# Kernel optimization log

Hardware: AMD Instinct MI355X
Metric: run time of the kernel (lower is better)

Reference implementation:

```python
import jax, jax.numpy as jnp
import numpy as np

D = H = W = 128  # voxel grid resolution (shape = [1,1,128,128,128] in source)
N = 2_000_000    # number of points


def splat(vals, pts, d, h, w):
    """Adjoint of trilinear F.grid_sample (align_corners=False, zeros padding).
    vals: [N] point values; pts: [N,3] normalized (x,y,z) coords in [-1,1].
    Returns [d,h,w] voxel grid with trilinear scatter-add of vals.
    """
    # unnormalize: pixel = ((coord+1)*size - 1) / 2  (align_corners=False)
    x = ((pts[:, 0] + 1.0) * w - 1.0) * 0.5
    y = ((pts[:, 1] + 1.0) * h - 1.0) * 0.5
    z = ((pts[:, 2] + 1.0) * d - 1.0) * 0.5
    x0 = jnp.floor(x); y0 = jnp.floor(y); z0 = jnp.floor(z)
    fx = x - x0; fy = y - y0; fz = z - z0
    x0i = x0.astype(jnp.int32); y0i = y0.astype(jnp.int32); z0i = z0.astype(jnp.int32)
    grid = jnp.zeros((d * h * w,), dtype=vals.dtype)
    for dz in (0, 1):
        wz = fz if dz else (1.0 - fz)
        for dy in (0, 1):
            wy = fy if dy else (1.0 - fy)
            for dx in (0, 1):
                wx = fx if dx else (1.0 - fx)
                xi = x0i + dx; yi = y0i + dy; zi = z0i + dz
                valid = (xi >= 0) & (xi < w) & (yi >= 0) & (yi < h) & (zi >= 0) & (zi < d)
                idx = jnp.where(valid, (zi * h + yi) * w + xi, 0)
                contrib = jnp.where(valid, wx * wy * wz * vals, 0.0)
                grid = grid.at[idx].add(contrib)
    return grid.reshape(d, h, w)


def huber_sum(pred, gt, delta=1.0):
    diff = pred - gt
    a = jnp.abs(diff)
    return jnp.sum(jnp.where(a <= delta, 0.5 * diff * diff, delta * (a - 0.5 * delta)))


def setup_inputs() -> dict:
    key = jax.random.key(0)
    k1, k2, k3 = jax.random.split(key, 3)
    coords = jax.random.uniform(k1, (1, N, 3), jnp.float32, -0.95, 0.95)
    registration_pred = 0.02 * jax.random.normal(k2, (1, N, 3), jnp.float32)
    registration_gt = 0.02 * jax.random.normal(k3, (1, N, 3), jnp.float32)
    return {"registration_pred": registration_pred,
            "registration_gt": registration_gt,
            "coords": coords}


def reference(registration_pred, registration_gt, coords):
    pred_pts = (coords + registration_pred).reshape(-1, 3)   # [N,3]
    gt_pts = (coords + registration_gt).reshape(-1, 3)       # [N,3]
    vals = jnp.ones((pred_pts.shape[0],), dtype=coords.dtype)
    pred_rast = splat(vals, pred_pts, D, H, W)   # [128,128,128]
    gt_rast = splat(vals, gt_pts, D, H, W)       # [128,128,128]
    return huber_sum(pred_rast, gt_rast)
```

## Files before the change

kernel.cpp:

```cpp
#include <hip/hip_runtime.h>
#include <stdint.h>

constexpr int GRID_R = 128;
constexpr int NVOX = GRID_R * GRID_R * GRID_R;

constexpr int TILE = 16;
constexpr int TPD = GRID_R / TILE;
constexpr int NBINS = TPD * TPD * TPD;
constexpr int CAP = 12288;
constexpr int CUR_STRIDE = 16;
constexpr size_t CUR_BYTES = (size_t)NBINS * CUR_STRIDE * sizeof(uint32_t);
constexpr size_t ITEMS_BYTES = (size_t)NBINS * CAP * sizeof(uint2);
constexpr size_t SORT_WS_NEEDED = CUR_BYTES + ITEMS_BYTES;

constexpr int PAD = 18;

constexpr int QXB = 9;
constexpr int QZSTRIDE = QXB * QXB;
constexpr int QARR = PAD * QZSTRIDE;
constexpr float QSCALE = 1024.0f;

__device__ __forceinline__ int axis_tiles(int c0, int* ts, int* ls) {
    int n = 0;
    if ((unsigned)c0 < (unsigned)GRID_R) {
        int tx = c0 >> 4; ts[0] = tx; ls[0] = c0 - (tx << 4); n = 1;
    }
    int c1 = c0 + 1;
    if ((unsigned)c1 < (unsigned)GRID_R) {
        int tx = c1 >> 4;
        if (!n || tx != ts[0]) { ts[n] = tx; ls[n] = c0 - (tx << 4); ++n; }
    }
    return n;
}

template <typename F>
__device__ __forceinline__ void for_each_replica(float px, float py, float pz,
                                                 uint32_t g, F&& emit) {
    float x0f = floorf(px), y0f = floorf(py), z0f = floorf(pz);
    int x0 = (int)x0f, y0 = (int)y0f, z0 = (int)z0f;
    float fx = px - x0f, fy = py - y0f, fz = pz - z0f;

    int txs[2], lxs[2], tys[2], lys[2], tzs[2], lzs[2];
    int ntx = axis_tiles(x0, txs, lxs);
    int nty = axis_tiles(y0, tys, lys);
    int ntz = axis_tiles(z0, tzs, lzs);
    if (!ntx || !nty || !ntz) return;

    uint32_t ufx = (uint32_t)(fx * 65535.0f + 0.5f);
    uint32_t ufy = (uint32_t)(fy * 65535.0f + 0.5f);
    uint32_t ufz = (uint32_t)(fz * 65535.0f + 0.5f);
    uint32_t w0 = ufx | (ufy << 16);

    for (int c = 0; c < ntz; ++c)
        for (int b = 0; b < nty; ++b)
            for (int a = 0; a < ntx; ++a) {
                int bin = (tzs[c] * TPD + tys[b]) * TPD + txs[a];
                uint32_t w1 = ufz |
                              ((uint32_t)(lxs[a] + 1) << 16) |
                              ((uint32_t)(lys[b] + 1) << 21) |
                              ((uint32_t)(lzs[c] + 1) << 26) |
                              (g << 31);
                emit(bin, w0, w1);
            }
}

__device__ __forceinline__ void load_pts(const float* __restrict__ pred_reg,
                                         const float* __restrict__ gt_reg,
                                         const float* __restrict__ coords,
                                         int i, float* pa, float* pb) {
    float cx = coords[3 * i + 0], cy = coords[3 * i + 1], cz = coords[3 * i + 2];
    pa[0] = (cx + pred_reg[3 * i + 0] + 1.0f) * 64.0f - 0.5f;
    pa[1] = (cy + pred_reg[3 * i + 1] + 1.0f) * 64.0f - 0.5f;
    pa[2] = (cz + pred_reg[3 * i + 2] + 1.0f) * 64.0f - 0.5f;
    pb[0] = (cx + gt_reg[3 * i + 0] + 1.0f) * 64.0f - 0.5f;
    pb[1] = (cy + gt_reg[3 * i + 1] + 1.0f) * 64.0f - 0.5f;
    pb[2] = (cz + gt_reg[3 * i + 2] + 1.0f) * 64.0f - 0.5f;
}

#define SBLOCK 1024
#define PPT 8

__global__ __launch_bounds__(SBLOCK, 8) void scatter_kernel(
        const float* __restrict__ pred_reg, const float* __restrict__ gt_reg,
        const float* __restrict__ coords, uint32_t* __restrict__ cursors,
        uint2* __restrict__ items, int n) {
    __shared__ uint32_t h[NBINS];
    __shared__ uint32_t base[NBINS];
    int t = threadIdx.x;
    for (int b = t; b < NBINS; b += SBLOCK) h[b] = 0;
    __syncthreads();

    int i0 = blockIdx.x * (SBLOCK * PPT);

    for (int k = 0; k < PPT; ++k) {
        int i = i0 + k * SBLOCK + t;
        if (i >= n) break;
        float pa[3], pb[3];
        load_pts(pred_reg, gt_reg, coords, i, pa, pb);
        auto cnt = [&](int bin, uint32_t, uint32_t) { atomicAdd(&h[bin], 1u); };
        for_each_replica(pa[0], pa[1], pa[2], 0u, cnt);
        for_each_replica(pb[0], pb[1], pb[2], 1u, cnt);
    }
    __syncthreads();

    for (int b = t; b < NBINS; b += SBLOCK) {
        uint32_t c = h[b];
        base[b] = c ? atomicAdd(&cursors[b * CUR_STRIDE], c) : 0u;
        h[b] = 0;
    }
    __syncthreads();

    for (int k = 0; k < PPT; ++k) {
        int i = i0 + k * SBLOCK + t;
        if (i >= n) break;
        float pa[3], pb[3];
        load_pts(pred_reg, gt_reg, coords, i, pa, pb);
        auto put = [&](int bin, uint32_t w0, uint32_t w1) {
            uint32_t r = atomicAdd(&h[bin], 1u);
            uint32_t s = base[bin] + r;
            if (s < (uint32_t)CAP)
                items[(size_t)bin * CAP + s] = make_uint2(w0, w1);
        };
        for_each_replica(pa[0], pa[1], pa[2], 0u, put);
        for_each_replica(pb[0], pb[1], pb[2], 1u, put);
    }
}

#define ABLOCK 1024

__device__ __forceinline__ void accum_item(uint64_t* __restrict__ U,
                                           uint32_t wx, uint32_t wy) {
    float fx = (float)(wx & 0xffffu) * (1.0f / 65535.0f);
    float fy = (float)(wx >> 16) * (1.0f / 65535.0f);
    float fz = (float)(wy & 0xffffu) * (1.0f / 65535.0f);
    int lx1 = (int)((wy >> 16) & 31u);
    int ly1 = (int)((wy >> 21) & 31u);
    int lz1 = (int)((wy >> 26) & 31u);
    uint32_t g = wy >> 31;

    int px = lx1 & 1, xb = lx1 >> 1;
    int py = ly1 & 1, yb = ly1 >> 1;
    uint64_t* arr = U + ((g << 2) | (py << 1) | px) * QARR;
    int idx = lz1 * QZSTRIDE + yb * QXB + xb;

    float wx1 = fx, wx0 = 1.0f - fx;
    float wy1 = fy, wy0 = 1.0f - fy;
    float q00 = wx0 * wy0 * QSCALE, q10 = wx1 * wy0 * QSCALE;
    float q01 = wx0 * wy1 * QSCALE, q11 = wx1 * wy1 * QSCALE;
    float wz1 = fz, wz0 = 1.0f - fz;

    auto pk = [&](float wz) -> uint64_t {
        uint32_t lo = (uint32_t)(q00 * wz + 0.5f) |
                      ((uint32_t)(q10 * wz + 0.5f) << 16);
        uint32_t hi = (uint32_t)(q01 * wz + 0.5f) |
                      ((uint32_t)(q11 * wz + 0.5f) << 16);
        return (uint64_t)lo | ((uint64_t)hi << 32);
    };
    atomicAdd((unsigned long long*)&arr[idx],
              (unsigned long long)pk(wz0));
    atomicAdd((unsigned long long*)&arr[idx + QZSTRIDE],
              (unsigned long long)pk(wz1));
}

__global__ __launch_bounds__(ABLOCK, 4) void accum_kernel(
        const uint2* __restrict__ items, const uint32_t* __restrict__ cursors,
        float* __restrict__ out) {
    __shared__ uint64_t U[8 * QARR];
    __shared__ float wsum[ABLOCK / 64];
    int bin = blockIdx.x, t = threadIdx.x;

    for (int j = t; j < 8 * QARR; j += ABLOCK) U[j] = 0ull;
    __syncthreads();

    uint32_t cnt = cursors[bin * CUR_STRIDE];
    if (cnt > (uint32_t)CAP) cnt = CAP;
    const uint2* seg = items + (size_t)bin * CAP;
    const uint4* seg4 = (const uint4*)seg;
    uint32_t npair = cnt >> 1;

    uint32_t i = t;
    uint4 w = (i < npair) ? seg4[i] : make_uint4(0, 0, 0, 0);
    while (i < npair) {
        uint32_t inext = i + ABLOCK;
        uint4 wn = (inext < npair) ? seg4[inext] : make_uint4(0, 0, 0, 0);
        accum_item(U, w.x, w.y);
        accum_item(U, w.z, w.w);
        w = wn; i = inext;
    }
    if ((cnt & 1) && t == 0) {
        uint2 lw = seg[cnt - 1];
        accum_item(U, lw.x, lw.y);
    }
    __syncthreads();

    float s = 0.0f;
    for (int j = t; j < TILE * TILE * TILE; j += ABLOCK) {
        int x = (j & 15) + 1, y = ((j >> 4) & 15) + 1, z = (j >> 8) + 1;
        float v[2];
#pragma unroll
        for (int g = 0; g < 2; ++g) {
            float acc = 0.0f;
#pragma unroll
            for (int py = 0; py < 2; ++py)
#pragma unroll
                for (int px = 0; px < 2; ++px) {
                    int xb = (x - px) >> 1, lx = (x - px) & 1;
                    int yb = (y - py) >> 1, ly = (y - py) & 1;
                    uint64_t q = U[((g << 2) | (py << 1) | px) * QARR +
                                   z * QZSTRIDE + yb * QXB + xb];
                    acc += (float)((uint32_t)(q >> (((ly << 1) | lx) << 4)) &
                                   0xFFFFu);
                }
            v[g] = acc;
        }
        float d = (v[0] - v[1]) * (1.0f / QSCALE);
        float aa = fabsf(d);
        s += (aa <= 1.0f) ? 0.5f * d * d : (aa - 0.5f);
    }
#pragma unroll
    for (int off = 32; off > 0; off >>= 1) s += __shfl_down(s, off, 64);
    int lane = t & 63, wid = t >> 6;
    if (!lane) wsum[wid] = s;
    __syncthreads();
    if (!t) {
        float tot = 0.0f;
#pragma unroll
        for (int wv = 0; wv < ABLOCK / 64; ++wv) tot += wsum[wv];
        unsafeAtomicAdd(out, tot);
    }
}

__device__ __forceinline__ void splat_point(float nx, float ny, float nz,
                                            float* __restrict__ grid) {
    float x = (nx + 1.0f) * 64.0f - 0.5f;
    float y = (ny + 1.0f) * 64.0f - 0.5f;
    float z = (nz + 1.0f) * 64.0f - 0.5f;
    float x0f = floorf(x), y0f = floorf(y), z0f = floorf(z);
    float fx = x - x0f, fy = y - y0f, fz = z - z0f;
    int x0 = (int)x0f, y0 = (int)y0f, z0 = (int)z0f;
    int xs[2] = {x0, x0 + 1}, ys[2] = {y0, y0 + 1}, zs[2] = {z0, z0 + 1};
    float wxs[2] = {1.0f - fx, fx}, wys[2] = {1.0f - fy, fy}, wzs[2] = {1.0f - fz, fz};
#pragma unroll
    for (int dz = 0; dz < 2; ++dz) {
        int zi = zs[dz]; if ((unsigned)zi >= (unsigned)GRID_R) continue;
#pragma unroll
        for (int dy = 0; dy < 2; ++dy) {
            int yi = ys[dy]; if ((unsigned)yi >= (unsigned)GRID_R) continue;
            float wzy = wzs[dz] * wys[dy];
            int basei = (zi * GRID_R + yi) * GRID_R;
#pragma unroll
            for (int dx = 0; dx < 2; ++dx) {
                int xi = xs[dx]; if ((unsigned)xi >= (unsigned)GRID_R) continue;
                unsafeAtomicAdd(&grid[basei + xi], wzy * wxs[dx]);
            }
        }
    }
}

__global__ void splat_kernel(const float* __restrict__ pred_reg,
                             const float* __restrict__ gt_reg,
                             const float* __restrict__ coords,
                             float* __restrict__ gridA, float* __restrict__ gridB,
                             int n) {
    int i = blockIdx.x * blockDim.x + threadIdx.x;
    if (i >= n) return;
    float cx = coords[3 * i + 0], cy = coords[3 * i + 1], cz = coords[3 * i + 2];
    splat_point(cx + pred_reg[3 * i + 0], cy + pred_reg[3 * i + 1],
                cz + pred_reg[3 * i + 2], gridA);
    splat_point(cx + gt_reg[3 * i + 0], cy + gt_reg[3 * i + 1],
                cz + gt_reg[3 * i + 2], gridB);
}

__global__ void huber_kernel(const float4* __restrict__ A,
                             const float4* __restrict__ B,
                             float* __restrict__ out) {
    int i = blockIdx.x * blockDim.x + threadIdx.x;
    float4 a = A[i], b = B[i];
    auto h1 = [](float d) { float x = fabsf(d);
                            return (x <= 1.0f) ? 0.5f * d * d : (x - 0.5f); };
    float s = h1(a.x - b.x) + h1(a.y - b.y) + h1(a.z - b.z) + h1(a.w - b.w);
#pragma unroll
    for (int off = 32; off > 0; off >>= 1) s += __shfl_down(s, off, 64);
    __shared__ float wsum[4];
    int lane = threadIdx.x & 63, wid = threadIdx.x >> 6;
    if (!lane) wsum[wid] = s;
    __syncthreads();
    if (!threadIdx.x) atomicAdd(out, wsum[0] + wsum[1] + wsum[2] + wsum[3]);
}

extern "C" void kernel_launch(void* const* d_in, const int* in_sizes, int n_in,
                              void* d_out, int out_size, void* d_ws, size_t ws_size,
                              hipStream_t stream) {
    const float* pred_reg = (const float*)d_in[0];
    const float* gt_reg   = (const float*)d_in[1];
    const float* coords   = (const float*)d_in[2];
    float* outp = (float*)d_out;
    int n = in_sizes[2] / 3;

    hipMemsetAsync(d_out, 0, sizeof(float), stream);

    if (ws_size >= SORT_WS_NEEDED) {
        uint32_t* cursors = (uint32_t*)d_ws;
        uint2* items = (uint2*)((char*)d_ws + CUR_BYTES);
        hipMemsetAsync(cursors, 0, CUR_BYTES, stream);

        int sblocks = (n + SBLOCK * PPT - 1) / (SBLOCK * PPT);
        scatter_kernel<<<sblocks, SBLOCK, 0, stream>>>(pred_reg, gt_reg, coords,
                                                       cursors, items, n);
        accum_kernel<<<NBINS, ABLOCK, 0, stream>>>(items, cursors, outp);
    } else {
        float* gridA = (float*)d_ws;
        float* gridB = gridA + NVOX;
        hipMemsetAsync(d_ws, 0, (size_t)2 * NVOX * sizeof(float), stream);
        int blocks = (n + 255) / 256;
        splat_kernel<<<blocks, 256, 0, stream>>>(pred_reg, gt_reg, coords,
                                                 gridA, gridB, n);
        huber_kernel<<<NVOX / 4 / 256, 256, 0, stream>>>((const float4*)gridA,
                                                         (const float4*)gridB, outp);
    }
}
```

Before: 170.9 us.

## Replace two-pass count/scatter binning with single-pass shared ring buffers flushed in groups

The scatter kernel no longer reads points twice (count pass then put pass). Each bin now gets a small shared-memory ring, and full groups of 8 items are flushed to global memory with one cursor atomic per group. Partial groups are padded with sentinel items, which the accumulation step skips, and bin capacity is raised to hold the padding. This removes the second point load and the per-block histogram pass, at the cost of extra syncs per iteration, global atomics on ring overflow, and lower occupancy from the larger shared-memory footprint.

```diff
diff --git a/kernel.cpp b/kernel.cpp
--- a/kernel.cpp
+++ b/kernel.cpp
@@ -7,11 +7,13 @@
 constexpr int TILE = 16;
 constexpr int TPD = GRID_R / TILE;
 constexpr int NBINS = TPD * TPD * TPD;
-constexpr int CAP = 12288;
+constexpr int CAP = 13312;
 constexpr int CUR_STRIDE = 16;
 constexpr size_t CUR_BYTES = (size_t)NBINS * CUR_STRIDE * sizeof(uint32_t);
 constexpr size_t ITEMS_BYTES = (size_t)NBINS * CAP * sizeof(uint2);
 constexpr size_t SORT_WS_NEEDED = CUR_BYTES + ITEMS_BYTES;
+
+constexpr uint32_t SENT_W1 = 0xFFFFFFFFu;
 
 constexpr int PAD = 18;
 
@@ -79,50 +81,83 @@
 
 #define SBLOCK 1024
 #define PPT 8
-
-__global__ __launch_bounds__(SBLOCK, 8) void scatter_kernel(
+constexpr int RCAP = 16;
+
+__global__ __launch_bounds__(SBLOCK) void scatter_kernel(
         const float* __restrict__ pred_reg, const float* __restrict__ gt_reg,
         const float* __restrict__ coords, uint32_t* __restrict__ cursors,
         uint2* __restrict__ items, int n) {
-    __shared__ uint32_t h[NBINS];
-    __shared__ uint32_t base[NBINS];
+    __shared__ uint2 ring[NBINS * RCAP];
+    __shared__ uint32_t pc[NBINS];
+    __shared__ uint32_t fl[NBINS];
     int t = threadIdx.x;
-    for (int b = t; b < NBINS; b += SBLOCK) h[b] = 0;
+    if (t < NBINS) { pc[t] = 0; fl[t] = 0; }
     __syncthreads();
 
     int i0 = blockIdx.x * (SBLOCK * PPT);
 
     for (int k = 0; k < PPT; ++k) {
         int i = i0 + k * SBLOCK + t;
-        if (i >= n) break;
-        float pa[3], pb[3];
-        load_pts(pred_reg, gt_reg, coords, i, pa, pb);
-        auto cnt = [&](int bin, uint32_t, uint32_t) { atomicAdd(&h[bin], 1u); };
-        for_each_replica(pa[0], pa[1], pa[2], 0u, cnt);
-        for_each_replica(pb[0], pb[1], pb[2], 1u, cnt);
-    }
-    __syncthreads();
-
-    for (int b = t; b < NBINS; b += SBLOCK) {
-        uint32_t c = h[b];
-        base[b] = c ? atomicAdd(&cursors[b * CUR_STRIDE], c) : 0u;
-        h[b] = 0;
-    }
-    __syncthreads();
-
-    for (int k = 0; k < PPT; ++k) {
-        int i = i0 + k * SBLOCK + t;
-        if (i >= n) break;
-        float pa[3], pb[3];
-        load_pts(pred_reg, gt_reg, coords, i, pa, pb);
-        auto put = [&](int bin, uint32_t w0, uint32_t w1) {
-            uint32_t r = atomicAdd(&h[bin], 1u);
-            uint32_t s = base[bin] + r;
-            if (s < (uint32_t)CAP)
-                items[(size_t)bin * CAP + s] = make_uint2(w0, w1);
-        };
-        for_each_replica(pa[0], pa[1], pa[2], 0u, put);
-        for_each_replica(pb[0], pb[1], pb[2], 1u, put);
+        if (i < n) {
+            float pa[3], pb[3];
+            load_pts(pred_reg, gt_reg, coords, i, pa, pb);
+            auto emit = [&](int bin, uint32_t w0, uint32_t w1) {
+                uint32_t base = fl[bin] * 8u;
+                uint32_t r = atomicAdd(&pc[bin], 1u);
+                if (r - base < (uint32_t)RCAP) {
+                    ring[bin * RCAP + (int)(r & (RCAP - 1))] = make_uint2(w0, w1);
+                } else {
+                    atomicSub(&pc[bin], 1u);
+                    uint32_t s = atomicAdd(&cursors[bin * CUR_STRIDE], 1u);
+                    if (s < (uint32_t)CAP)
+                        items[(size_t)bin * CAP + s] = make_uint2(w0, w1);
+                }
+            };
+            for_each_replica(pa[0], pa[1], pa[2], 0u, emit);
+            for_each_replica(pb[0], pb[1], pb[2], 1u, emit);
+        }
+        __syncthreads();
+        if (t < NBINS) {
+            uint32_t f = fl[t], p = pc[t];
+            uint32_t ng = (p - f * 8u) >> 3;
+            if (ng) {
+                uint32_t s0 = atomicAdd(&cursors[t * CUR_STRIDE], ng * 8u);
+                for (uint32_t g = 0; g < ng; ++g) {
+                    uint32_t sb = s0 + g * 8u;
+                    int rb = t * RCAP + (int)(((f + g) & 1u) << 3);
+                    uint2* dst = items + (size_t)t * CAP + sb;
+                    if (sb + 8u <= (uint32_t)CAP) {
+#pragma unroll
+                        for (int j = 0; j < 8; ++j) dst[j] = ring[rb + j];
+                    } else {
+                        for (int j = 0; j < 8; ++j)
+                            if (sb + j < (uint32_t)CAP) dst[j] = ring[rb + j];
+                    }
+                }
+                fl[t] = f + ng;
+            }
+        }
+        __syncthreads();
+    }
+
+    if (t < NBINS) {
+        uint32_t f = fl[t], p = pc[t];
+        uint32_t res = p - f * 8u;
+        if (res) {
+            for (uint32_t j = res; j < 8u; ++j)
+                ring[t * RCAP + (int)((f * 8u + j) & (RCAP - 1))] =
+                    make_uint2(0u, SENT_W1);
+            uint32_t s0 = atomicAdd(&cursors[t * CUR_STRIDE], 8u);
+            int rb = t * RCAP + (int)((f & 1u) << 3);
+            uint2* dst = items + (size_t)t * CAP + s0;
+            if (s0 + 8u <= (uint32_t)CAP) {
+#pragma unroll
+                for (int j = 0; j < 8; ++j) dst[j] = ring[rb + j];
+            } else {
+                for (int j = 0; j < 8; ++j)
+                    if (s0 + j < (uint32_t)CAP) dst[j] = ring[rb + j];
+            }
+        }
     }
 }
 
@@ -130,10 +165,11 @@
 
 __device__ __forceinline__ void accum_item(uint64_t* __restrict__ U,
                                            uint32_t wx, uint32_t wy) {
+    int lx1 = (int)((wy >> 16) & 31u);
+    if (lx1 == 31) return;
     float fx = (float)(wx & 0xffffu) * (1.0f / 65535.0f);
     float fy = (float)(wx >> 16) * (1.0f / 65535.0f);
     float fz = (float)(wy & 0xffffu) * (1.0f / 65535.0f);
-    int lx1 = (int)((wy >> 16) & 31u);
     int ly1 = (int)((wy >> 21) & 31u);
     int lz1 = (int)((wy >> 26) & 31u);
     uint32_t g = wy >> 31;
```

Measured after the change: 169.2 us. Within noise of the previous version (-1.0%).

## Stage scatter writes through per-bin LDS ring buffers for coalesced 64-byte flushes

Applied to the files above, without the earlier changes.

The binning scatter kernel now buffers items in a 16-entry shared-memory ring per bin and flushes full groups of 8 items as 64-byte vector stores, instead of each thread doing a scattered 8-byte global store. Per-bin reservations are rounded up to multiples of 16, and leftover slots are padded with sentinel items that the accumulate kernel skips. Ring overflow goes to a small per-bin spill region read separately. This aims to cut write inefficiency from scattered stores, at the cost of extra block-wide barriers per PPT iteration, more shared memory (lower occupancy), larger capacity and sentinel padding traffic.

```diff
diff --git a/kernel.cpp b/kernel.cpp
--- a/kernel.cpp
+++ b/kernel.cpp
@@ -7,11 +7,15 @@
 constexpr int TILE = 16;
 constexpr int TPD = GRID_R / TILE;
 constexpr int NBINS = TPD * TPD * TPD;
-constexpr int CAP = 12288;
+constexpr int CAP = 13312;
+constexpr int SPILL_CAP = 64;
+constexpr int CAPM = CAP - SPILL_CAP;
 constexpr int CUR_STRIDE = 16;
 constexpr size_t CUR_BYTES = (size_t)NBINS * CUR_STRIDE * sizeof(uint32_t);
 constexpr size_t ITEMS_BYTES = (size_t)NBINS * CAP * sizeof(uint2);
 constexpr size_t SORT_WS_NEEDED = CUR_BYTES + ITEMS_BYTES;
+
+constexpr uint32_t SENT_W1 = 0xFFFFFFFFu;
 
 constexpr int PAD = 18;
 
@@ -79,15 +83,19 @@
 
 #define SBLOCK 1024
 #define PPT 8
-
-__global__ __launch_bounds__(SBLOCK, 8) void scatter_kernel(
+constexpr int RCAP = 16;
+
+__global__ __launch_bounds__(SBLOCK) void scatter_kernel(
         const float* __restrict__ pred_reg, const float* __restrict__ gt_reg,
         const float* __restrict__ coords, uint32_t* __restrict__ cursors,
         uint2* __restrict__ items, int n) {
+    __shared__ alignas(16) uint2 ring[NBINS * RCAP];
     __shared__ uint32_t h[NBINS];
     __shared__ uint32_t base[NBINS];
+    __shared__ uint32_t rsv[NBINS];
+    __shared__ uint32_t fl[NBINS];
     int t = threadIdx.x;
-    for (int b = t; b < NBINS; b += SBLOCK) h[b] = 0;
+    if (t < NBINS) h[t] = 0;
     __syncthreads();
 
     int i0 = blockIdx.x * (SBLOCK * PPT);
@@ -103,26 +111,83 @@
     }
     __syncthreads();
 
-    for (int b = t; b < NBINS; b += SBLOCK) {
-        uint32_t c = h[b];
-        base[b] = c ? atomicAdd(&cursors[b * CUR_STRIDE], c) : 0u;
-        h[b] = 0;
+    if (t < NBINS) {
+        uint32_t c = h[t];
+        uint32_t r = (c + 15u) & ~15u;
+        base[t] = r ? atomicAdd(&cursors[t * CUR_STRIDE], r) : 0u;
+        rsv[t] = r;
+        h[t] = 0;
+        fl[t] = 0;
     }
     __syncthreads();
 
     for (int k = 0; k < PPT; ++k) {
         int i = i0 + k * SBLOCK + t;
-        if (i >= n) break;
-        float pa[3], pb[3];
-        load_pts(pred_reg, gt_reg, coords, i, pa, pb);
-        auto put = [&](int bin, uint32_t w0, uint32_t w1) {
-            uint32_t r = atomicAdd(&h[bin], 1u);
-            uint32_t s = base[bin] + r;
-            if (s < (uint32_t)CAP)
-                items[(size_t)bin * CAP + s] = make_uint2(w0, w1);
-        };
-        for_each_replica(pa[0], pa[1], pa[2], 0u, put);
-        for_each_replica(pb[0], pb[1], pb[2], 1u, put);
+        if (i < n) {
+            float pa[3], pb[3];
+            load_pts(pred_reg, gt_reg, coords, i, pa, pb);
+            auto emit = [&](int bin, uint32_t w0, uint32_t w1) {
+                uint32_t fb = fl[bin] * 8u;
+                uint32_t r = atomicAdd(&h[bin], 1u);
+                if (r - fb < (uint32_t)RCAP) {
+                    ring[bin * RCAP + (int)(r & (RCAP - 1))] = make_uint2(w0, w1);
+                } else {
+                    atomicSub(&h[bin], 1u);
+                    uint32_t s = atomicAdd(&cursors[bin * CUR_STRIDE + 1], 1u);
+                    if (s < (uint32_t)SPILL_CAP)
+                        items[(size_t)bin * CAP + CAPM + s] = make_uint2(w0, w1);
+                }
+            };
+            for_each_replica(pa[0], pa[1], pa[2], 0u, emit);
+            for_each_replica(pb[0], pb[1], pb[2], 1u, emit);
+        }
+        __syncthreads();
+        if (t < NBINS) {
+            uint32_t f = fl[t], p = h[t];
+            uint32_t ng = (p - f * 8u) >> 3;
+            if (ng) {
+                const uint4* rsrc = (const uint4*)&ring[t * RCAP];
+                for (uint32_t g = 0; g < ng; ++g) {
+                    uint32_t sb = base[t] + (f + g) * 8u;
+                    if (sb + 8u <= (uint32_t)CAPM) {
+                        uint4* dst = (uint4*)(items + (size_t)t * CAP + sb);
+                        const uint4* src = rsrc + ((int)((f + g) & 1u)) * 4;
+                        dst[0] = src[0]; dst[1] = src[1];
+                        dst[2] = src[2]; dst[3] = src[3];
+                    }
+                }
+                fl[t] = f + ng;
+            }
+        }
+        __syncthreads();
+    }
+
+    if (t < NBINS) {
+        uint32_t f = fl[t], p = h[t];
+        uint32_t fi = f * 8u;
+        if (p > fi) {
+            for (uint32_t j = p; j < fi + 8u; ++j)
+                ring[t * RCAP + (int)(j & (RCAP - 1))] = make_uint2(0u, SENT_W1);
+            uint32_t sb = base[t] + fi;
+            if (sb + 8u <= (uint32_t)CAPM) {
+                uint4* dst = (uint4*)(items + (size_t)t * CAP + sb);
+                const uint4* src = (const uint4*)&ring[t * RCAP] +
+                                   ((int)(f & 1u)) * 4;
+                dst[0] = src[0]; dst[1] = src[1];
+                dst[2] = src[2]; dst[3] = src[3];
+            }
+            fi += 8u;
+        }
+        uint32_t reserved = rsv[t];
+        uint4 sent = make_uint4(0u, SENT_W1, 0u, SENT_W1);
+        while (fi < reserved) {
+            uint32_t sb = base[t] + fi;
+            if (sb + 8u <= (uint32_t)CAPM) {
+                uint4* dst = (uint4*)(items + (size_t)t * CAP + sb);
+                dst[0] = sent; dst[1] = sent; dst[2] = sent; dst[3] = sent;
+            }
+            fi += 8u;
+        }
     }
 }
 
@@ -130,10 +195,11 @@
 
 __device__ __forceinline__ void accum_item(uint64_t* __restrict__ U,
                                            uint32_t wx, uint32_t wy) {
+    int lx1 = (int)((wy >> 16) & 31u);
+    if (lx1 == 31) return;
     float fx = (float)(wx & 0xffffu) * (1.0f / 65535.0f);
     float fy = (float)(wx >> 16) * (1.0f / 65535.0f);
     float fz = (float)(wy & 0xffffu) * (1.0f / 65535.0f);
-    int lx1 = (int)((wy >> 16) & 31u);
     int ly1 = (int)((wy >> 21) & 31u);
     int lz1 = (int)((wy >> 26) & 31u);
     uint32_t g = wy >> 31;
@@ -173,7 +239,9 @@
     __syncthreads();
 
     uint32_t cnt = cursors[bin * CUR_STRIDE];
-    if (cnt > (uint32_t)CAP) cnt = CAP;
+    if (cnt > (uint32_t)CAPM) cnt = CAPM;
+    uint32_t sc = cursors[bin * CUR_STRIDE + 1];
+    if (sc > (uint32_t)SPILL_CAP) sc = SPILL_CAP;
     const uint2* seg = items + (size_t)bin * CAP;
     const uint4* seg4 = (const uint4*)seg;
     uint32_t npair = cnt >> 1;
@@ -189,6 +257,10 @@
     }
     if ((cnt & 1) && t == 0) {
         uint2 lw = seg[cnt - 1];
+        accum_item(U, lw.x, lw.y);
+    }
+    for (uint32_t j = t; j < sc; j += ABLOCK) {
+        uint2 lw = seg[CAPM + j];
         accum_item(U, lw.x, lw.y);
     }
     __syncthreads();
```

Result: slower. 183.5 us (+7.4%).
